# Kernel optimization log

Measured on AMD Instinct MI355X. Metric: run time of the kernel, lower is better.

The kernel has to match this reference:

```python
import jax, jax.numpy as jnp
import numpy as np

B, F, E, H, L = 64, 512, 256, 8, 4  # batch, feature_dim(seq), embed_dim, heads, layers
D = E // H                          # head dim = 32


def setup_inputs() -> dict:
    key = jax.random.key(0)
    ks = jax.random.split(key, 12)
    def w(k, shape, fan_in):
        return jax.random.normal(k, shape, jnp.float32) / np.sqrt(fan_in)
    return {
        "features": jax.random.normal(ks[0], (B, F), jnp.float32),
        "emb_w": w(ks[1], (1, E), 1), "emb_b": w(ks[2], (E,), 1),
        "q_w": w(ks[3], (E, E), E), "q_b": w(ks[4], (E,), E),
        "k_w": w(ks[5], (E, E), E), "k_b": w(ks[6], (E,), E),
        "v_w": w(ks[7], (E, E), E), "v_b": w(ks[8], (E,), E),
        "attn_w": w(ks[9], (E, 1), E), "attn_b": w(ks[10], (1,), E),
    }


def reference(features, emb_w, emb_b, q_w, q_b, k_w, k_b, v_w, v_b, attn_w, attn_b):
    # features: [B, F] -> per-feature scalar embedded to E dims
    emb = features[..., None] @ emb_w + emb_b          # [B, F, E]
    # Q path: input is zeros -> embedding gives emb_b, then query linear; constant per position
    q_vec = emb_b @ q_w + q_b                          # [E]
    Q = jnp.broadcast_to(q_vec, (B, F, E)).reshape(B, F, H, D).transpose(0, 2, 1, 3)  # [B,H,F,D]
    K = (emb @ k_w + k_b).reshape(B, F, H, D).transpose(0, 2, 1, 3)
    V = (emb @ v_w + v_b).reshape(B, F, H, D).transpose(0, 2, 1, 3)
    scale = 1.0 / np.sqrt(D)
    v_sum = V.sum(axis=2, keepdims=True)               # [B,H,1,D]; ones@V row-sums
    Qc = Qnc = Q
    for _ in range(L):
        A = jax.nn.softmax(jnp.einsum('bhfd,bhgd->bhfg', Q, K) * scale, axis=-1)
        Qc = jnp.einsum('bhfg,bhgd->bhfd', A, V)       # A @ V
        Qnc = v_sum - Qc                                # (1 - A) @ V, identical math
        Q = Qc
    def merge(t):
        return t.transpose(0, 2, 1, 3).reshape(B, F, E)
    h_ox = (merge(Qc) @ attn_w + attn_b)[..., 0]       # [B, F]
    h_c = (merge(Qnc) @ attn_w + attn_b)[..., 0]       # [B, F]
    return (h_ox, h_c)
```

## Files before the change

### kernel.cpp

```cpp
#include <hip/hip_runtime.h>

#define BB 64
#define FF 512
#define EE 256
#define HH 8
#define DD 32
#define LL 4

__global__ __launch_bounds__(256) void tm_fused_kernel(
    const float* __restrict__ x,
    const float* __restrict__ emb_w,
    const float* __restrict__ emb_b,
    const float* __restrict__ q_w,
    const float* __restrict__ q_b,
    const float* __restrict__ k_w,
    const float* __restrict__ k_b,
    const float* __restrict__ v_w,
    const float* __restrict__ v_b,
    const float* __restrict__ attn_w,
    const float* __restrict__ attn_b,
    float* __restrict__ out)
{
    const int tid = threadIdx.x;
    const int b = blockIdx.x;

    __shared__ float s_ew[EE], s_eb[EE];
    __shared__ float s_a0[HH], s_c1[HH], s_c2[HH], s_p1[HH], s_p0[HH];
    __shared__ float s_m[HH];
    __shared__ float s_hox, s_hc;

    s_ew[tid] = emb_w[tid];
    s_eb[tid] = emb_b[tid];
    __syncthreads();

    float kw = 0.f, kb = 0.f, vw = 0.f, vb = 0.f, qv = 0.f;
    for (int j = 0; j < EE; ++j) {
        const float ew = s_ew[j], eb = s_eb[j];
        const float kwe = k_w[j * EE + tid];
        const float vwe = v_w[j * EE + tid];
        const float qwe = q_w[j * EE + tid];
        kw = fmaf(ew, kwe, kw);
        kb = fmaf(eb, kwe, kb);
        vw = fmaf(ew, vwe, vw);
        vb = fmaf(eb, vwe, vb);
        qv = fmaf(eb, qwe, qv);
    }
    kb += k_b[tid];
    vb += v_b[tid];
    qv += q_b[tid];
    const float aw = attn_w[tid];

    const float scale = 0.17677669529663687f;

    float t0 = qv * kw;
    float t1 = vw * kw;
    float t2 = vb * kw;
    float t3 = vw * aw;
    float t4 = vb * aw;
    for (int off = 16; off > 0; off >>= 1) {
        t0 += __shfl_xor(t0, off, 32);
        t1 += __shfl_xor(t1, off, 32);
        t2 += __shfl_xor(t2, off, 32);
        t3 += __shfl_xor(t3, off, 32);
        t4 += __shfl_xor(t4, off, 32);
    }
    if ((tid & 31) == 0) {
        const int h = tid >> 5;
        s_a0[h] = t0 * scale;
        s_c1[h] = t1;
        s_c2[h] = t2;
        s_p1[h] = t3;
        s_p0[h] = t4;
    }
    __syncthreads();

    const int h = tid >> 5;
    const int lane = tid & 31;

    float xr[16];
    #pragma unroll
    for (int k = 0; k < 16; ++k)
        xr[k] = x[b * FF + lane + 32 * k];

    float sx = 0.f;
    #pragma unroll
    for (int k = 0; k < 16; ++k) sx += xr[k];
    for (int off = 16; off > 0; off >>= 1) sx += __shfl_xor(sx, off, 32);

    float a = s_a0[h];
    const float c1 = s_c1[h], c2 = s_c2[h];
    float m = 0.f;
    for (int it = 0; it < LL; ++it) {
        float mx = -3.4e38f;
        #pragma unroll
        for (int k = 0; k < 16; ++k) mx = fmaxf(mx, a * xr[k]);
        for (int off = 16; off > 0; off >>= 1) mx = fmaxf(mx, __shfl_xor(mx, off, 32));
        float s0 = 0.f, s1 = 0.f;
        #pragma unroll
        for (int k = 0; k < 16; ++k) {
            const float e = __expf(fmaf(a, xr[k], -mx));
            s0 += e;
            s1 = fmaf(e, xr[k], s1);
        }
        for (int off = 16; off > 0; off >>= 1) {
            s0 += __shfl_xor(s0, off, 32);
            s1 += __shfl_xor(s1, off, 32);
        }
        m = s1 / s0;
        a = scale * fmaf(m, c1, c2);
    }
    if (lane == 0) s_m[h] = m;
    __syncthreads();

    if (tid == 0) {
        const float ab = attn_b[0];
        float hox = ab, hc = ab;
        for (int hh = 0; hh < HH; ++hh) {
            const float qc = fmaf(s_m[hh], s_p1[hh], s_p0[hh]);
            hox += qc;
            hc += fmaf(sx, s_p1[hh], (float)FF * s_p0[hh]) - qc;
        }
        s_hox = hox;
        s_hc = hc;
    }
    __syncthreads();

    const float hox = s_hox, hc = s_hc;
    out[b * FF + tid]                 = hox;
    out[b * FF + tid + 256]           = hox;
    out[BB * FF + b * FF + tid]       = hc;
    out[BB * FF + b * FF + tid + 256] = hc;
}

extern "C" void kernel_launch(void* const* d_in, const int* in_sizes, int n_in,
                              void* d_out, int out_size, void* d_ws, size_t ws_size,
                              hipStream_t stream) {
    const float* features = (const float*)d_in[0];
    const float* emb_w    = (const float*)d_in[1];
    const float* emb_b    = (const float*)d_in[2];
    const float* q_w      = (const float*)d_in[3];
    const float* q_b      = (const float*)d_in[4];
    const float* k_w      = (const float*)d_in[5];
    const float* k_b      = (const float*)d_in[6];
    const float* v_w      = (const float*)d_in[7];
    const float* v_b      = (const float*)d_in[8];
    const float* attn_w   = (const float*)d_in[9];
    const float* attn_b   = (const float*)d_in[10];
    float* out = (float*)d_out;

    tm_fused_kernel<<<dim3(BB), dim3(256), 0, stream>>>(
        features, emb_w, emb_b, q_w, q_b, k_w, k_b, v_w, v_b, attn_w, attn_b, out);
}
```

Baseline: 90.19 us.

## Vectorize weight projection loads with float4 and split-K reduction through shared memory

The weight-folding loop now has each thread load float4 slices of k_w/v_w/q_w over a quarter of the rows. The four partial sums per column are then reduced through a new shared buffer, cutting the number of serial global loads per thread fourfold. Feature loads are also vectorized to float4, and the softmax logits are cached so they are not recomputed. This adds about 20KB of shared memory and an extra barrier. The feature permutation does not change the results, because only the sums are used.

```diff
diff --git a/kernel.cpp b/kernel.cpp
--- a/kernel.cpp
+++ b/kernel.cpp
@@ -23,28 +23,51 @@
 {
     const int tid = threadIdx.x;
     const int b = blockIdx.x;
+    const int g = tid >> 6;
+    const int c = (tid & 63) << 2;
 
     __shared__ float s_ew[EE], s_eb[EE];
-    __shared__ float s_a0[HH], s_c1[HH], s_c2[HH], s_p1[HH], s_p0[HH];
-    __shared__ float s_m[HH];
+    __shared__ float s_red[5][4 * EE];
+    __shared__ float s_a0[HH], s_c1[HH], s_c2[HH], s_p1[HH], s_p0[HH], s_m[HH];
     __shared__ float s_hox, s_hc;
 
     s_ew[tid] = emb_w[tid];
     s_eb[tid] = emb_b[tid];
     __syncthreads();
 
-    float kw = 0.f, kb = 0.f, vw = 0.f, vb = 0.f, qv = 0.f;
-    for (int j = 0; j < EE; ++j) {
+    float4 kw4 = {0,0,0,0}, kb4 = {0,0,0,0}, vw4 = {0,0,0,0},
+           vb4 = {0,0,0,0}, qv4 = {0,0,0,0};
+    #pragma unroll 4
+    for (int j4 = 0; j4 < 64; ++j4) {
+        const int j = (j4 << 2) + g;
         const float ew = s_ew[j], eb = s_eb[j];
-        const float kwe = k_w[j * EE + tid];
-        const float vwe = v_w[j * EE + tid];
-        const float qwe = q_w[j * EE + tid];
-        kw = fmaf(ew, kwe, kw);
-        kb = fmaf(eb, kwe, kb);
-        vw = fmaf(ew, vwe, vw);
-        vb = fmaf(eb, vwe, vb);
-        qv = fmaf(eb, qwe, qv);
+        const float4 K = *(const float4*)(k_w + j * EE + c);
+        const float4 V = *(const float4*)(v_w + j * EE + c);
+        const float4 Q = *(const float4*)(q_w + j * EE + c);
+        kw4.x = fmaf(ew, K.x, kw4.x); kw4.y = fmaf(ew, K.y, kw4.y);
+        kw4.z = fmaf(ew, K.z, kw4.z); kw4.w = fmaf(ew, K.w, kw4.w);
+        kb4.x = fmaf(eb, K.x, kb4.x); kb4.y = fmaf(eb, K.y, kb4.y);
+        kb4.z = fmaf(eb, K.z, kb4.z); kb4.w = fmaf(eb, K.w, kb4.w);
+        vw4.x = fmaf(ew, V.x, vw4.x); vw4.y = fmaf(ew, V.y, vw4.y);
+        vw4.z = fmaf(ew, V.z, vw4.z); vw4.w = fmaf(ew, V.w, vw4.w);
+        vb4.x = fmaf(eb, V.x, vb4.x); vb4.y = fmaf(eb, V.y, vb4.y);
+        vb4.z = fmaf(eb, V.z, vb4.z); vb4.w = fmaf(eb, V.w, vb4.w);
+        qv4.x = fmaf(eb, Q.x, qv4.x); qv4.y = fmaf(eb, Q.y, qv4.y);
+        qv4.z = fmaf(eb, Q.z, qv4.z); qv4.w = fmaf(eb, Q.w, qv4.w);
     }
+    const int ri = (g << 8) + c;
+    *(float4*)&s_red[0][ri] = kw4;
+    *(float4*)&s_red[1][ri] = kb4;
+    *(float4*)&s_red[2][ri] = vw4;
+    *(float4*)&s_red[3][ri] = vb4;
+    *(float4*)&s_red[4][ri] = qv4;
+    __syncthreads();
+
+    float kw = s_red[0][tid] + s_red[0][256 + tid] + s_red[0][512 + tid] + s_red[0][768 + tid];
+    float kb = s_red[1][tid] + s_red[1][256 + tid] + s_red[1][512 + tid] + s_red[1][768 + tid];
+    float vw = s_red[2][tid] + s_red[2][256 + tid] + s_red[2][512 + tid] + s_red[2][768 + tid];
+    float vb = s_red[3][tid] + s_red[3][256 + tid] + s_red[3][512 + tid] + s_red[3][768 + tid];
+    float qv = s_red[4][tid] + s_red[4][256 + tid] + s_red[4][512 + tid] + s_red[4][768 + tid];
     kb += k_b[tid];
     vb += v_b[tid];
     qv += q_b[tid];
@@ -79,8 +102,11 @@
 
     float xr[16];
     #pragma unroll
-    for (int k = 0; k < 16; ++k)
-        xr[k] = x[b * FF + lane + 32 * k];
+    for (int k = 0; k < 4; ++k) {
+        const float4 xv = *(const float4*)(x + b * FF + (lane << 2) + (k << 7));
+        xr[4 * k + 0] = xv.x; xr[4 * k + 1] = xv.y;
+        xr[4 * k + 2] = xv.z; xr[4 * k + 3] = xv.w;
+    }
 
     float sx = 0.f;
     #pragma unroll
@@ -91,14 +117,18 @@
     const float c1 = s_c1[h], c2 = s_c2[h];
     float m = 0.f;
     for (int it = 0; it < LL; ++it) {
+        float p[16];
         float mx = -3.4e38f;
         #pragma unroll
-        for (int k = 0; k < 16; ++k) mx = fmaxf(mx, a * xr[k]);
+        for (int k = 0; k < 16; ++k) {
+            p[k] = a * xr[k];
+            mx = fmaxf(mx, p[k]);
+        }
         for (int off = 16; off > 0; off >>= 1) mx = fmaxf(mx, __shfl_xor(mx, off, 32));
         float s0 = 0.f, s1 = 0.f;
         #pragma unroll
         for (int k = 0; k < 16; ++k) {
-            const float e = __expf(fmaf(a, xr[k], -mx));
+            const float e = __expf(p[k] - mx);
             s0 += e;
             s1 = fmaf(e, xr[k], s1);
         }
```

Result: faster. 86.77 us (-3.8%).
